# Optimization experiments

Measured on AMD Instinct MI355X. Metric: run time of the kernel, lower is better.

The kernel has to match this reference:

```python
import jax, jax.numpy as jnp
import numpy as np

L1, L2, N, C = 4096, 4096, 8, 3


def setup_inputs() -> dict:
    key = jax.random.key(0)
    k1, k2 = jax.random.split(key)
    coords1 = jax.random.uniform(k1, (L1, N, C), dtype=jnp.float32)
    coords2 = jax.random.uniform(k2, (L2, N, C), dtype=jnp.float32)
    return {"coords1": coords1, "coords2": coords2}


def reference(coords1, coords2):
    # coords1: [L1, N, C], coords2: [L2, N, C]
    l1, n, c = coords1.shape
    l2 = coords2.shape[0]
    # Batch-first layout, matching flatten_batch semantics (per-batch NN only)
    q = jnp.swapaxes(coords2, 0, 1)  # [N, L2, C] query points
    r = jnp.swapaxes(coords1, 0, 1)  # [N, L1, C] reference points
    # Squared euclidean distances per batch: [N, L2, L1]
    d2 = (
        jnp.sum(q * q, axis=-1)[:, :, None]
        + jnp.sum(r * r, axis=-1)[:, None, :]
        - 2.0 * jnp.einsum("nlc,nmc->nlm", q, r)
    )
    # tc.nearest returns global flat index; original does fmod(L1) to get the
    # per-batch index — argmin within each batch gives that directly.
    nearest = jnp.argmin(d2, axis=-1)  # [N, L2]
    clusters = nearest.T  # [L2, N]
    # torch.meshgrid(arange(L2), arange(N)) with 'ij' indexing; indices[-1] is
    # the batch index broadcast to [L2, N].
    batch_idx = jnp.broadcast_to(jnp.arange(n, dtype=jnp.int64 if False else jnp.int32), (l2, n))
    return (clusters.reshape(-1), batch_idx.reshape(-1))
```

## Files before the change

kernel.cpp:

```cpp
#include <hip/hip_runtime.h>
#include <float.h>


typedef float v2f __attribute__((ext_vector_type(2)));

constexpr int kL1 = 4096, kL2 = 4096, kN = 8;
constexpr int kChunk = 2048;
constexpr int kQ = 8;
constexpr int kQPerBlock = 32;

__global__ __launch_bounds__(256, 4)
void nearest_kernel(const float* __restrict__ c1, const float* __restrict__ c2,
                    int* __restrict__ out) {
#pragma clang fp contract(off)
  __shared__ float4 refs[kChunk];

  const int tid = threadIdx.x;
  const int n = blockIdx.y;
  const int wave = tid >> 6;
  const int lane = tid & 63;
  const int q0 = blockIdx.x * kQPerBlock + wave * kQ;

  v2f qx[4], qy[4], qz[4], qq[4];
#pragma unroll
  for (int i = 0; i < 4; ++i) {
    const float* p0 = c2 + ((q0 + 2 * i) * kN + n) * 3;
    const float* p1 = c2 + ((q0 + 2 * i + 1) * kN + n) * 3;
    const float a0 = p0[0], a1 = p0[1], a2 = p0[2];
    const float b0 = p1[0], b1 = p1[1], b2 = p1[2];
    qx[i] = v2f{a0, b0};
    qy[i] = v2f{a1, b1};
    qz[i] = v2f{a2, b2};
    qq[i] = v2f{
        __fadd_rn(__fadd_rn(__fmul_rn(a0, a0), __fmul_rn(a1, a1)),
                  __fmul_rn(a2, a2)),
        __fadd_rn(__fadd_rn(__fmul_rn(b0, b0), __fmul_rn(b1, b1)),
                  __fmul_rn(b2, b2))};
  }

  v2f bd[4];
  int bi[kQ];
#pragma unroll
  for (int i = 0; i < 4; ++i) { bd[i] = v2f{FLT_MAX, FLT_MAX}; }
#pragma unroll
  for (int i = 0; i < kQ; ++i) { bi[i] = 0; }

  for (int chunk = 0; chunk < kL1 / kChunk; ++chunk) {
    __syncthreads();

#pragma unroll
    for (int k = 0; k < kChunk / 256; ++k) {
      const int j = tid + 256 * k;
      const float* p = c1 + ((chunk * kChunk + j) * kN + n) * 3;
      const float r0 = p[0], r1 = p[1], r2 = p[2];
      const float rr = __fadd_rn(
          __fadd_rn(__fmul_rn(r0, r0), __fmul_rn(r1, r1)), __fmul_rn(r2, r2));
      refs[j] = make_float4(r0, r1, r2, rr);
    }
    __syncthreads();

    const int base = chunk * kChunk + lane;
#pragma unroll 2
    for (int t = 0; t < kChunk / 64; ++t) {
      const float4 r = refs[lane + 64 * t];
      const int j = base + 64 * t;
#pragma unroll
      for (int i = 0; i < 4; ++i) {
        const v2f m0 = qx[i] * r.x;
        const v2f m1 = qy[i] * r.y;
        const v2f s01 = m0 + m1;
        const v2f m2 = qz[i] * r.z;
        const v2f dot = s01 + m2;
        const v2f A = qq[i] + r.w;
        const float da = __fmaf_rn(-2.0f, dot.x, A.x);
        const float db = __fmaf_rn(-2.0f, dot.y, A.y);
        if (da < bd[i].x) { bd[i].x = da; bi[2 * i] = j; }
        if (db < bd[i].y) { bd[i].y = db; bi[2 * i + 1] = j; }
      }
    }
  }

  float d[kQ];
#pragma unroll
  for (int i = 0; i < 4; ++i) { d[2 * i] = bd[i].x; d[2 * i + 1] = bd[i].y; }

#pragma unroll
  for (int i = 0; i < kQ; ++i) {
#pragma unroll
    for (int m = 1; m <= 32; m <<= 1) {
      const float od = __shfl_xor(d[i], m);
      const int oi = __shfl_xor(bi[i], m);
      if (od < d[i] || (od == d[i] && oi < bi[i])) { d[i] = od; bi[i] = oi; }
    }
  }

  if (lane == 0) {
#pragma unroll
    for (int i = 0; i < kQ; ++i) {
      out[(q0 + i) * kN + n] = bi[i];
      out[kL2 * kN + (q0 + i) * kN + n] = n;
    }
  }
}

extern "C" void kernel_launch(void* const* d_in, const int* in_sizes, int n_in,
                              void* d_out, int out_size, void* d_ws, size_t ws_size,
                              hipStream_t stream) {
  const float* c1 = (const float*)d_in[0];
  const float* c2 = (const float*)d_in[1];
  int* out = (int*)d_out;
  dim3 grid(kL2 / kQPerBlock, kN);
  nearest_kernel<<<grid, dim3(256), 0, stream>>>(c1, c2, out);
}
```

Baseline: 94.80 us.

## Split reference set across blocks with partial argmin and separate merge kernel

Restructures the nearest-neighbor search so each block handles 128 queries for all 8 batches against a slice of the reference points, writing per-slice (distance, index) partials to workspace. A second kernel merges the partials per query. Packed f32 math is forced through inline v_pk_* asm, and references are stored pair-interleaved in LDS. This raises parallelism and removes the wave-level shuffle reduction, at the cost of an extra launch and workspace traffic.

```diff
diff --git a/kernel.cpp b/kernel.cpp
--- a/kernel.cpp
+++ b/kernel.cpp
@@ -4,103 +4,117 @@
 
 typedef float v2f __attribute__((ext_vector_type(2)));
 
+__device__ __forceinline__ v2f pk_mul(v2f a, v2f b) {
+  v2f d; asm("v_pk_mul_f32 %0, %1, %2" : "=v"(d) : "v"(a), "v"(b)); return d;
+}
+__device__ __forceinline__ v2f pk_add(v2f a, v2f b) {
+  v2f d; asm("v_pk_add_f32 %0, %1, %2" : "=v"(d) : "v"(a), "v"(b)); return d;
+}
+__device__ __forceinline__ v2f pk_fma(v2f a, v2f b, v2f c) {
+  v2f d; asm("v_pk_fma_f32 %0, %1, %2, %3" : "=v"(d) : "v"(a), "v"(b), "v"(c)); return d;
+}
+
 constexpr int kL1 = 4096, kL2 = 4096, kN = 8;
-constexpr int kChunk = 2048;
-constexpr int kQ = 8;
-constexpr int kQPerBlock = 32;
+constexpr int kNStrideV2 = 260;
 
 __global__ __launch_bounds__(256, 4)
-void nearest_kernel(const float* __restrict__ c1, const float* __restrict__ c2,
-                    int* __restrict__ out) {
+void nn_partial(const float* __restrict__ c1, const float* __restrict__ c2,
+                uint2* __restrict__ part, int refsPerBlock) {
 #pragma clang fp contract(off)
-  __shared__ float4 refs[kChunk];
+  __shared__ v2f lds[8 * kNStrideV2];
 
   const int tid = threadIdx.x;
-  const int n = blockIdx.y;
-  const int wave = tid >> 6;
-  const int lane = tid & 63;
-  const int q0 = blockIdx.x * kQPerBlock + wave * kQ;
+  const int bx = blockIdx.x;
+  const int by = blockIdx.y;
+  const int n = tid >> 5;
+  const int qlane = tid & 31;
 
   v2f qx[4], qy[4], qz[4], qq[4];
+  int qi[4];
 #pragma unroll
-  for (int i = 0; i < 4; ++i) {
-    const float* p0 = c2 + ((q0 + 2 * i) * kN + n) * 3;
-    const float* p1 = c2 + ((q0 + 2 * i + 1) * kN + n) * 3;
-    const float a0 = p0[0], a1 = p0[1], a2 = p0[2];
-    const float b0 = p1[0], b1 = p1[1], b2 = p1[2];
-    qx[i] = v2f{a0, b0};
-    qy[i] = v2f{a1, b1};
-    qz[i] = v2f{a2, b2};
-    qq[i] = v2f{
-        __fadd_rn(__fadd_rn(__fmul_rn(a0, a0), __fmul_rn(a1, a1)),
-                  __fmul_rn(a2, a2)),
-        __fadd_rn(__fadd_rn(__fmul_rn(b0, b0), __fmul_rn(b1, b1)),
-                  __fmul_rn(b2, b2))};
+  for (int k = 0; k < 4; ++k) {
+    qi[k] = bx * 128 + qlane + 32 * k;
+    const float* p = c2 + (qi[k] * kN + n) * 3;
+    const float a0 = p[0], a1 = p[1], a2 = p[2];
+    const float s = __fadd_rn(
+        __fadd_rn(__fmul_rn(a0, a0), __fmul_rn(a1, a1)), __fmul_rn(a2, a2));
+    qx[k] = v2f{a0, a0}; qy[k] = v2f{a1, a1};
+    qz[k] = v2f{a2, a2}; qq[k] = v2f{s, s};
   }
+  const v2f cm2 = {-2.0f, -2.0f};
 
-  v2f bd[4];
-  int bi[kQ];
+  float bd[4]; int bi[4];
 #pragma unroll
-  for (int i = 0; i < 4; ++i) { bd[i] = v2f{FLT_MAX, FLT_MAX}; }
+  for (int k = 0; k < 4; ++k) { bd[k] = FLT_MAX; bi[k] = 0; }
+
+  const int refBase = by * refsPerBlock;
+  for (int c = 0; c < refsPerBlock; c += 128) {
+    __syncthreads();
 #pragma unroll
-  for (int i = 0; i < kQ; ++i) { bi[i] = 0; }
-
-  for (int chunk = 0; chunk < kL1 / kChunk; ++chunk) {
-    __syncthreads();
-
-#pragma unroll
-    for (int k = 0; k < kChunk / 256; ++k) {
-      const int j = tid + 256 * k;
-      const float* p = c1 + ((chunk * kChunk + j) * kN + n) * 3;
-      const float r0 = p[0], r1 = p[1], r2 = p[2];
-      const float rr = __fadd_rn(
-          __fadd_rn(__fmul_rn(r0, r0), __fmul_rn(r1, r1)), __fmul_rn(r2, r2));
-      refs[j] = make_float4(r0, r1, r2, rr);
+    for (int tk = 0; tk < 2; ++tk) {
+      const int id = tid + 256 * tk;
+      const int pn = id & 7;
+      const int pp = id >> 3;
+      const int j0 = refBase + c + 2 * pp;
+      const float* r0 = c1 + (j0 * kN + pn) * 3;
+      const float* r1 = c1 + ((j0 + 1) * kN + pn) * 3;
+      const float x0 = r0[0], y0 = r0[1], z0 = r0[2];
+      const float x1 = r1[0], y1 = r1[1], z1 = r1[2];
+      const float rr0 = __fadd_rn(
+          __fadd_rn(__fmul_rn(x0, x0), __fmul_rn(y0, y0)), __fmul_rn(z0, z0));
+      const float rr1 = __fadd_rn(
+          __fadd_rn(__fmul_rn(x1, x1), __fmul_rn(y1, y1)), __fmul_rn(z1, z1));
+      v2f* dst = lds + pn * kNStrideV2 + pp * 4;
+      dst[0] = v2f{x0, x1}; dst[1] = v2f{y0, y1};
+      dst[2] = v2f{z0, z1}; dst[3] = v2f{rr0, rr1};
     }
     __syncthreads();
 
-    const int base = chunk * kChunk + lane;
-#pragma unroll 2
-    for (int t = 0; t < kChunk / 64; ++t) {
-      const float4 r = refs[lane + 64 * t];
-      const int j = base + 64 * t;
+    const int jb = refBase + c;
+    const v2f* row = lds + n * kNStrideV2;
+#pragma unroll 4
+    for (int p = 0; p < 64; ++p) {
+      const v2f x2 = row[p * 4 + 0];
+      const v2f y2 = row[p * 4 + 1];
+      const v2f z2 = row[p * 4 + 2];
+      const v2f w2 = row[p * 4 + 3];
+      const int j0 = jb + 2 * p;
 #pragma unroll
-      for (int i = 0; i < 4; ++i) {
-        const v2f m0 = qx[i] * r.x;
-        const v2f m1 = qy[i] * r.y;
-        const v2f s01 = m0 + m1;
-        const v2f m2 = qz[i] * r.z;
-        const v2f dot = s01 + m2;
-        const v2f A = qq[i] + r.w;
-        const float da = __fmaf_rn(-2.0f, dot.x, A.x);
-        const float db = __fmaf_rn(-2.0f, dot.y, A.y);
-        if (da < bd[i].x) { bd[i].x = da; bi[2 * i] = j; }
-        if (db < bd[i].y) { bd[i].y = db; bi[2 * i + 1] = j; }
+      for (int k = 0; k < 4; ++k) {
+        const v2f m0 = pk_mul(qx[k], x2);
+        const v2f m1 = pk_mul(qy[k], y2);
+        const v2f s01 = pk_add(m0, m1);
+        const v2f m2 = pk_mul(qz[k], z2);
+        const v2f dot = pk_add(s01, m2);
+        const v2f A = pk_add(qq[k], w2);
+        const v2f d2 = pk_fma(dot, cm2, A);
+        if (d2.x < bd[k]) { bd[k] = d2.x; bi[k] = j0; }
+        if (d2.y < bd[k]) { bd[k] = d2.y; bi[k] = j0 + 1; }
       }
     }
   }
 
-  float d[kQ];
 #pragma unroll
-  for (int i = 0; i < 4; ++i) { d[2 * i] = bd[i].x; d[2 * i + 1] = bd[i].y; }
+  for (int k = 0; k < 4; ++k) {
+    part[((by * 8 + n) * 4096) + qi[k]] =
+        make_uint2(__float_as_uint(bd[k]), (unsigned)bi[k]);
+  }
+}
 
-#pragma unroll
-  for (int i = 0; i < kQ; ++i) {
-#pragma unroll
-    for (int m = 1; m <= 32; m <<= 1) {
-      const float od = __shfl_xor(d[i], m);
-      const int oi = __shfl_xor(bi[i], m);
-      if (od < d[i] || (od == d[i] && oi < bi[i])) { d[i] = od; bi[i] = oi; }
-    }
+__global__ __launch_bounds__(256)
+void nn_merge(const uint2* __restrict__ part, int* __restrict__ out, int R) {
+  const int id = blockIdx.x * 256 + threadIdx.x;
+  const int n = id >> 12;
+  const int qi = id & 4095;
+  float bd = FLT_MAX; int bi = 0;
+  for (int r = 0; r < R; ++r) {
+    const uint2 v = part[(r * 8 + n) * 4096 + qi];
+    const float d = __uint_as_float(v.x);
+    const int i = (int)v.y;
+    if (d < bd || (d == bd && i < bi)) { bd = d; bi = i; }
   }
-
-  if (lane == 0) {
-#pragma unroll
-    for (int i = 0; i < kQ; ++i) {
-      out[(q0 + i) * kN + n] = bi[i];
-      out[kL2 * kN + (q0 + i) * kN + n] = n;
-    }
-  }
+  out[qi * kN + n] = bi;
+  out[kL2 * kN + qi * kN + n] = n;
 }
 
 extern "C" void kernel_launch(void* const* d_in, const int* in_sizes, int n_in,
@@ -109,6 +123,11 @@
   const float* c1 = (const float*)d_in[0];
   const float* c2 = (const float*)d_in[1];
   int* out = (int*)d_out;
-  dim3 grid(kL2 / kQPerBlock, kN);
-  nearest_kernel<<<grid, dim3(256), 0, stream>>>(c1, c2, out);
+
+  int R = 32;
+  while (R > 1 && (size_t)R * 8 * 4096 * sizeof(uint2) > ws_size) R >>= 1;
+  const int refsPerBlock = kL1 / R;
+
+  nn_partial<<<dim3(32, R), 256, 0, stream>>>(c1, c2, (uint2*)d_ws, refsPerBlock);
+  nn_merge<<<dim3(32768 / 256), 256, 0, stream>>>((const uint2*)d_ws, out, R);
 }
```

New measurement: 97.60 us. 3.0% more time.
